# Kernel tuning notes

Hardware: AMD Instinct MI355X
Metric: run time of the kernel (lower is better)

Reference implementation:

```python
import jax, jax.numpy as jnp
import numpy as np

B, S, D = 8, 2048, 1024
TEMPERATURE = 32.0  # sqrt(d_model)
NEG_INF = -1e16


def setup_inputs() -> dict:
    key = jax.random.key(0)
    ks = jax.random.split(key, 9)
    sc = 1.0 / np.sqrt(D)
    q = jax.random.normal(ks[0], (B, S, D), dtype=jnp.float32)
    k = jax.random.normal(ks[1], (B, S, D), dtype=jnp.float32)
    v = jax.random.normal(ks[2], (B, S, D), dtype=jnp.float32)
    # nn.Linear weights are [out, in]; init roughly uniform(-1/sqrt(in), 1/sqrt(in))
    Wq = jax.random.uniform(ks[3], (D, D), jnp.float32, -sc, sc)
    Wk = jax.random.uniform(ks[4], (D, D), jnp.float32, -sc, sc)
    Wv = jax.random.uniform(ks[5], (D, D), jnp.float32, -sc, sc)
    bq = jax.random.uniform(ks[6], (D,), jnp.float32, -sc, sc)
    bk = jax.random.uniform(ks[7], (D,), jnp.float32, -sc, sc)
    bv = jax.random.uniform(ks[8], (D,), jnp.float32, -sc, sc)
    # causal mask: True where attention is DISALLOWED (masked_fill semantics)
    mask = jnp.triu(jnp.ones((S, S), dtype=bool), k=1)
    mask = jnp.broadcast_to(mask[None, :, :], (B, S, S))
    return {"q": q, "k": k, "v": v, "Wq": Wq, "bq": bq, "Wk": Wk,
            "bk": bk, "Wv": Wv, "bv": bv, "mask": mask}


def reference(q, k, v, Wq, bq, Wk, bk, Wv, bv, mask):
    # Linear projections (torch Linear: x @ W.T + b)
    qp = jnp.einsum('bsd,ed->bse', q, Wq) + bq  # [B,S,D]
    kp = jnp.einsum('bsd,ed->bse', k, Wk) + bk
    vp = jnp.einsum('bsd,ed->bse', v, Wv) + bv
    # scores [B,S,S]
    attn = jnp.einsum('bsd,btd->bst', qp, kp) / TEMPERATURE
    attn = jnp.where(mask, NEG_INF, attn)
    attn = jax.nn.softmax(attn, axis=2)
    # dropout p=0.0 -> identity (eval mode)
    output = jnp.einsum('bst,btd->bsd', attn, vp)  # [B,S,D]
    return (output, attn)
```

## Files before the change

### kernel.cpp

```cpp
#include <hip/hip_runtime.h>
#include <hip/hip_bf16.h>
#include <stdint.h>

#define SEQ 2048
#define DIM 1024
#define NB  8

typedef __attribute__((ext_vector_type(8))) __bf16 bf16x8;
typedef __attribute__((ext_vector_type(8))) unsigned short ushort8;
typedef __attribute__((ext_vector_type(4))) float f32x4;

__device__ inline unsigned short f2b(float f) {
  union { float f; uint32_t u; } c; c.f = f;
  uint32_t u = c.u;
  return (unsigned short)((u + 0x7fffu + ((u >> 16) & 1u)) >> 16);
}

__device__ inline void async16(const void* g, void* l) {
  __builtin_amdgcn_global_load_lds((const __attribute__((address_space(1))) uint32_t*)g,
                                   (__attribute__((address_space(3))) uint32_t*)l,
                                   16, 0, 0);
}

__global__ __launch_bounds__(256) void cvt_f32_bf16(const float* __restrict__ in,
                                                    unsigned short* __restrict__ out, int n4) {
  int idx = blockIdx.x * 256 + threadIdx.x;
  int stride = gridDim.x * 256;
  for (int i = idx; i < n4; i += stride) {
    float4 f = ((const float4*)in)[i];
    ushort4 h;
    h.x = f2b(f.x); h.y = f2b(f.y); h.z = f2b(f.z); h.w = f2b(f.w);
    ((ushort4*)out)[i] = h;
  }
}

template<int MODE>
__global__ __launch_bounds__(512, 2)
void gemm256(const unsigned short* __restrict__ A,
             const unsigned short* __restrict__ B,
             void* __restrict__ Cv,
             const float* __restrict__ bias,
             int K, int lda, int ldb, int ldc,
             long long aStride, long long bStride, long long cStride,
             float scale)
{
  extern __shared__ __align__(16) unsigned short lds[];
  unsigned short* const lA0 = lds;
  unsigned short* const lB0 = lds + 4 * 8192;

  const int mT = gridDim.x, nT = gridDim.y;
  const int nwg = mT * nT;
  const int did = blockIdx.y * mT + blockIdx.x;
  const int chunk = nwg >> 3;
  const int tile = (did & 7) * chunk + (did >> 3);
  const int bm = tile / nT;
  const int bn = tile % nT;
  if (MODE == 1 && bn > bm) return;
  const int bm0 = bm << 8;
  const int bn0 = bn << 8;
  const int z = blockIdx.z;
  A += (long long)z * aStride;
  B += (long long)z * bStride;

  const int tid  = threadIdx.x;
  const int lane = tid & 63;
  const int wv   = tid >> 6;
  const int wm   = wv >> 2;
  const int wn   = wv & 3;
  const int l15  = lane & 15;
  const int l4   = lane >> 4;
  const int Keff = (MODE == 2) ? (bm0 + 256) : K;
  const int NT   = Keff >> 6;

  auto LAh = [&](int buf, int kh) { return lA0 + ((buf << 1) + kh) * 8192; };
  auto LBh = [&](int buf, int kh) { return lB0 + ((buf << 1) + kh) * 8192; };

  const int rS   = tid >> 2;
  const int cSrc = ((tid & 3) << 4) ^ ((rS & 3) << 4);
  const char* gA0 = (const char*)A + ((size_t)(bm0 + rS) * lda) * 2 + cSrc;
  const char* gA1 = gA0 + (size_t)128 * lda * 2;
  const char* gB0 = (const char*)B + ((size_t)(bn0 + rS) * ldb) * 2 + cSrc;
  const char* gB1 = gB0 + (size_t)128 * ldb * 2;

  auto stageA = [&](int buf, int t64, int kh) {
    size_t ko = (size_t)t64 * 128 + (size_t)(kh << 6);
    unsigned short* d = LAh(buf, kh);
    async16(gA0 + ko, d + tid * 8);
    async16(gA1 + ko, d + (tid + 512) * 8);
  };
  auto stageB = [&](int buf, int t64, int kh) {
    size_t ko = (size_t)t64 * 128 + (size_t)(kh << 6);
    unsigned short* d = LBh(buf, kh);
    async16(gB0 + ko, d + tid * 8);
    async16(gB1 + ko, d + (tid + 512) * 8);
  };

  const int swz = (l4 << 4) ^ ((l15 & 3) << 4);
  int aOff[8], bOff[4];
  #pragma unroll
  for (int m = 0; m < 8; ++m) aOff[m] = ((wm << 7) + (m << 4) + l15) * 64 + swz;
  #pragma unroll
  for (int n = 0; n < 4; ++n) bOff[n] = ((wn << 6) + (n << 4) + l15) * 64 + swz;

  auto rd = [&](const unsigned short* base, int off) -> bf16x8 {
    return __builtin_bit_cast(bf16x8, *(const ushort8*)((const char*)base + off));
  };

  f32x4 acc[8][4] = {};
  bf16x8 aF[8], bFa, bFb;

  stageA(0, 0, 0); stageB(0, 0, 0); stageA(0, 0, 1); stageB(0, 0, 1);
  stageA(1, 1, 0); stageB(1, 1, 0); stageA(1, 1, 1);
  asm volatile("s_waitcnt vmcnt(6)" ::: "memory");
  __builtin_amdgcn_s_barrier();
  __builtin_amdgcn_sched_barrier(0);

  for (int tt = 0; tt < NT; ++tt) {
    const int buf = tt & 1;
    const unsigned short* a0 = LAh(buf, 0);
    const unsigned short* a1 = LAh(buf, 1);
    const unsigned short* b0 = LBh(buf, 0);
    const unsigned short* b1 = LBh(buf, 1);

    #pragma unroll
    for (int m = 0; m < 8; ++m) aF[m] = rd(a0, aOff[m]);
    bFa = rd(b0, bOff[0]); bFb = rd(b0, bOff[1]);
    if (tt + 1 < NT) stageB(buf ^ 1, tt + 1, 1);
    __builtin_amdgcn_s_barrier();
    asm volatile("s_waitcnt lgkmcnt(0)" ::: "memory");
    __builtin_amdgcn_sched_barrier(0);
    __builtin_amdgcn_s_setprio(1);
    #pragma unroll
    for (int m = 0; m < 8; ++m) {
      acc[m][0] = __builtin_amdgcn_mfma_f32_16x16x32_bf16(aF[m], bFa, acc[m][0], 0, 0, 0);
      acc[m][1] = __builtin_amdgcn_mfma_f32_16x16x32_bf16(aF[m], bFb, acc[m][1], 0, 0, 0);
    }
    __builtin_amdgcn_s_setprio(0);
    __builtin_amdgcn_s_barrier();
    __builtin_amdgcn_sched_barrier(0);

    bFa = rd(b0, bOff[2]); bFb = rd(b0, bOff[3]);
    if (tt + 2 < NT) stageA(buf, tt + 2, 0);
    __builtin_amdgcn_s_barrier();
    asm volatile("s_waitcnt lgkmcnt(0)" ::: "memory");
    __builtin_amdgcn_sched_barrier(0);
    __builtin_amdgcn_s_setprio(1);
    #pragma unroll
    for (int m = 0; m < 8; ++m) {
      acc[m][2] = __builtin_amdgcn_mfma_f32_16x16x32_bf16(aF[m], bFa, acc[m][2], 0, 0, 0);
      acc[m][3] = __builtin_amdgcn_mfma_f32_16x16x32_bf16(aF[m], bFb, acc[m][3], 0, 0, 0);
    }
    __builtin_amdgcn_s_setprio(0);
    __builtin_amdgcn_s_barrier();
    __builtin_amdgcn_sched_barrier(0);

    #pragma unroll
    for (int m = 0; m < 8; ++m) aF[m] = rd(a1, aOff[m]);
    bFa = rd(b1, bOff[0]); bFb = rd(b1, bOff[1]);
    if (tt + 2 < NT) stageB(buf, tt + 2, 0);
    __builtin_amdgcn_s_barrier();
    asm volatile("s_waitcnt lgkmcnt(0)" ::: "memory");
    __builtin_amdgcn_sched_barrier(0);
    __builtin_amdgcn_s_setprio(1);
    #pragma unroll
    for (int m = 0; m < 8; ++m) {
      acc[m][0] = __builtin_amdgcn_mfma_f32_16x16x32_bf16(aF[m], bFa, acc[m][0], 0, 0, 0);
      acc[m][1] = __builtin_amdgcn_mfma_f32_16x16x32_bf16(aF[m], bFb, acc[m][1], 0, 0, 0);
    }
    __builtin_amdgcn_s_setprio(0);
    __builtin_amdgcn_s_barrier();
    __builtin_amdgcn_sched_barrier(0);

    bFa = rd(b1, bOff[2]); bFb = rd(b1, bOff[3]);
    if (tt + 2 < NT) stageA(buf, tt + 2, 1);
    __builtin_amdgcn_s_barrier();
    asm volatile("s_waitcnt lgkmcnt(0)" ::: "memory");
    __builtin_amdgcn_sched_barrier(0);
    __builtin_amdgcn_s_setprio(1);
    #pragma unroll
    for (int m = 0; m < 8; ++m) {
      acc[m][2] = __builtin_amdgcn_mfma_f32_16x16x32_bf16(aF[m], bFa, acc[m][2], 0, 0, 0);
      acc[m][3] = __builtin_amdgcn_mfma_f32_16x16x32_bf16(aF[m], bFb, acc[m][3], 0, 0, 0);
    }
    __builtin_amdgcn_s_setprio(0);
    if (tt + 2 < NT) asm volatile("s_waitcnt vmcnt(6)" ::: "memory");
    else             asm volatile("s_waitcnt vmcnt(0)" ::: "memory");
    __builtin_amdgcn_s_barrier();
    __builtin_amdgcn_sched_barrier(0);
  }

  if (MODE == 0) {
    unsigned short* Ch = (unsigned short*)Cv;
    float bvv[4];
    #pragma unroll
    for (int n = 0; n < 4; ++n) bvv[n] = bias[bn0 + (wn << 6) + (n << 4) + l15];
    #pragma unroll
    for (int m = 0; m < 8; ++m) {
      int rowb = bm0 + (wm << 7) + (m << 4) + (l4 << 2);
      #pragma unroll
      for (int r = 0; r < 4; ++r) {
        int row = rowb + r;
        #pragma unroll
        for (int n = 0; n < 4; ++n) {
          int col = bn0 + (wn << 6) + (n << 4) + l15;
          Ch[(size_t)row * ldc + col] = f2b(acc[m][n][r] + bvv[n]);
        }
      }
    }
  } else {
    float* Cf = (float*)Cv + (long long)z * cStride;
    #pragma unroll
    for (int m = 0; m < 8; ++m) {
      int rowb = bm0 + (wm << 7) + (m << 4) + (l4 << 2);
      #pragma unroll
      for (int r = 0; r < 4; ++r) {
        int row = rowb + r;
        #pragma unroll
        for (int n = 0; n < 4; ++n) {
          int col = bn0 + (wn << 6) + (n << 4) + l15;
          Cf[(size_t)row * ldc + col] = acc[m][n][r] * scale;
        }
      }
    }
  }
}

__global__ __launch_bounds__(256)
void softmax_causal(float* __restrict__ attnF, unsigned short* __restrict__ attnH) {
  const int S = SEQ;
  int row = blockIdx.x;
  int i = row & (S - 1);
  float* rp = attnF + (size_t)row * S;
  unsigned short* hp = attnH + (size_t)row * S;
  int len = i + 1;
  int tid = threadIdx.x;
  float vals[8];
  float m = -1e30f;
  #pragma unroll
  for (int it = 0; it < 8; ++it) {
    int j = it * 256 + tid;
    float v = (j < len) ? rp[j] : -1e30f;
    vals[it] = v;
    m = fmaxf(m, v);
  }
  #pragma unroll
  for (int o = 32; o > 0; o >>= 1) m = fmaxf(m, __shfl_xor(m, o, 64));
  __shared__ float red[4];
  int wv = tid >> 6, lane = tid & 63;
  if (lane == 0) red[wv] = m;
  __syncthreads();
  m = fmaxf(fmaxf(red[0], red[1]), fmaxf(red[2], red[3]));
  __syncthreads();
  float s = 0.f;
  #pragma unroll
  for (int it = 0; it < 8; ++it) {
    float e = __expf(vals[it] - m);
    vals[it] = e;
    s += e;
  }
  #pragma unroll
  for (int o = 32; o > 0; o >>= 1) s += __shfl_xor(s, o, 64);
  if (lane == 0) red[wv] = s;
  __syncthreads();
  s = red[0] + red[1] + red[2] + red[3];
  float inv = 1.f / s;
  #pragma unroll
  for (int it = 0; it < 8; ++it) {
    float o = vals[it] * inv;
    rp[it * 256 + tid] = o;
    hp[it * 256 + tid] = f2b(o);
  }
}

__global__ void transpose_bf16(const unsigned short* __restrict__ in, unsigned short* __restrict__ out) {
  __shared__ unsigned short tile[32][33];
  size_t zoff = (size_t)blockIdx.z * SEQ * DIM;
  const unsigned short* ip = in + zoff;
  unsigned short* op = out + zoff;
  int c0 = blockIdx.x * 32;
  int r0 = blockIdx.y * 32;
  int tx = threadIdx.x, ty = threadIdx.y;
  #pragma unroll
  for (int dy = 0; dy < 32; dy += 8)
    tile[ty + dy][tx] = ip[(size_t)(r0 + ty + dy) * DIM + c0 + tx];
  __syncthreads();
  #pragma unroll
  for (int dy = 0; dy < 32; dy += 8)
    op[(size_t)(c0 + ty + dy) * SEQ + r0 + tx] = tile[tx][ty + dy];
}

extern "C" void kernel_launch(void* const* d_in, const int* in_sizes, int n_in,
                              void* d_out, int out_size, void* d_ws, size_t ws_size,
                              hipStream_t stream) {
  (void)in_sizes; (void)n_in; (void)out_size; (void)ws_size;
  const int B = NB, S = SEQ, D = DIM;
  const size_t BSD = (size_t)B * S * D;
  const size_t DD  = (size_t)D * D;

  const float* q  = (const float*)d_in[0];
  const float* k  = (const float*)d_in[1];
  const float* v  = (const float*)d_in[2];
  const float* Wq = (const float*)d_in[3];
  const float* bq = (const float*)d_in[4];
  const float* Wk = (const float*)d_in[5];
  const float* bk = (const float*)d_in[6];
  const float* Wv = (const float*)d_in[7];
  const float* bv = (const float*)d_in[8];

  float* out   = (float*)d_out;
  float* attnF = out + BSD;

  unsigned short* xb  = (unsigned short*)d_ws;
  unsigned short* Wqb = xb + BSD;
  unsigned short* Wkb = Wqb + DD;
  unsigned short* Wvb = Wkb + DD;
  unsigned short* qp  = Wvb + DD;
  unsigned short* kp  = qp + BSD;
  unsigned short* vp  = kp + BSD;
  unsigned short* attnH = vp;

  static bool attrDone = []() {
    hipFuncSetAttribute(reinterpret_cast<const void*>(&gemm256<0>),
                        hipFuncAttributeMaxDynamicSharedMemorySize, 131072);
    hipFuncSetAttribute(reinterpret_cast<const void*>(&gemm256<1>),
                        hipFuncAttributeMaxDynamicSharedMemorySize, 131072);
    hipFuncSetAttribute(reinterpret_cast<const void*>(&gemm256<2>),
                        hipFuncAttributeMaxDynamicSharedMemorySize, 131072);
    return true;
  }();
  (void)attrDone;

  dim3 blk(256);
  dim3 gblk(512);
  const size_t GLDS = 131072;
  cvt_f32_bf16<<<dim3(512), blk, 0, stream>>>(Wq, Wqb, (int)(DD / 4));
  cvt_f32_bf16<<<dim3(512), blk, 0, stream>>>(Wk, Wkb, (int)(DD / 4));
  cvt_f32_bf16<<<dim3(512), blk, 0, stream>>>(Wv, Wvb, (int)(DD / 4));
  cvt_f32_bf16<<<dim3(4096), blk, 0, stream>>>(q, xb, (int)(BSD / 4));
  gemm256<0><<<dim3(64, 4, 1), gblk, GLDS, stream>>>(xb, Wqb, qp, bq, D, D, D, D, 0, 0, 0, 1.f);
  cvt_f32_bf16<<<dim3(4096), blk, 0, stream>>>(k, xb, (int)(BSD / 4));
  gemm256<0><<<dim3(64, 4, 1), gblk, GLDS, stream>>>(xb, Wkb, kp, bk, D, D, D, D, 0, 0, 0, 1.f);
  cvt_f32_bf16<<<dim3(4096), blk, 0, stream>>>(v, xb, (int)(BSD / 4));
  gemm256<0><<<dim3(64, 4, 1), gblk, GLDS, stream>>>(xb, Wvb, vp, bv, D, D, D, D, 0, 0, 0, 1.f);
  transpose_bf16<<<dim3(D / 32, S / 32, B), dim3(32, 8), 0, stream>>>(vp, xb);
  gemm256<1><<<dim3(S / 256, S / 256, B), gblk, GLDS, stream>>>(qp, kp, attnF, nullptr,
      D, D, D, S, (long long)S * D, (long long)S * D, (long long)S * S, 1.f / 32.f);
  softmax_causal<<<dim3(B * S), blk, 0, stream>>>(attnF, attnH);
  gemm256<2><<<dim3(S / 256, D / 256, B), gblk, GLDS, stream>>>(attnH, xb, out, nullptr,
      S, S, S, D, (long long)S * S, (long long)D * S, (long long)S * D, 1.f);
}
```

Before: 729.7 us.

## Batch QKV projections into one launch, restructure GEMM LDS reads, vectorize transpose

Merges the three weight conversions and the three input conversions into grid-y batched kernels. The three QKV projection GEMMs become a single z-batched launch with a per-z bias, provided the workspace is large enough. The GEMM inner loop now loads all four B fragments at once, dropping two of the four barrier/lgkmcnt wait points per k-step. The V transpose moves to 64x64 tiles with 16-byte vector accesses and an XOR-swizzled LDS tile. A fallback path keeps sequential projections for small workspaces. The tradeoffs are more registers per thread in the GEMM and a larger workspace requirement.

```diff
diff --git a/kernel.cpp b/kernel.cpp
--- a/kernel.cpp
+++ b/kernel.cpp
@@ -34,12 +34,30 @@
   }
 }
 
+__global__ __launch_bounds__(256) void cvt3_f32_bf16(const float* __restrict__ s0,
+                                                     const float* __restrict__ s1,
+                                                     const float* __restrict__ s2,
+                                                     unsigned short* __restrict__ out, int n4) {
+  const float* src = (blockIdx.y == 0) ? s0 : (blockIdx.y == 1) ? s1 : s2;
+  unsigned short* dst = out + (size_t)blockIdx.y * (size_t)n4 * 4;
+  int idx = blockIdx.x * 256 + threadIdx.x;
+  int stride = gridDim.x * 256;
+  for (int i = idx; i < n4; i += stride) {
+    float4 f = ((const float4*)src)[i];
+    ushort4 h;
+    h.x = f2b(f.x); h.y = f2b(f.y); h.z = f2b(f.z); h.w = f2b(f.w);
+    ((ushort4*)dst)[i] = h;
+  }
+}
+
 template<int MODE>
 __global__ __launch_bounds__(512, 2)
 void gemm256(const unsigned short* __restrict__ A,
              const unsigned short* __restrict__ B,
              void* __restrict__ Cv,
-             const float* __restrict__ bias,
+             const float* __restrict__ bias0,
+             const float* __restrict__ bias1,
+             const float* __restrict__ bias2,
              int K, int lda, int ldb, int ldc,
              long long aStride, long long bStride, long long cStride,
              float scale)
@@ -107,7 +125,7 @@
   };
 
   f32x4 acc[8][4] = {};
-  bf16x8 aF[8], bFa, bFb;
+  bf16x8 aF[8], bF[4];
 
   stageA(0, 0, 0); stageB(0, 0, 0); stageA(0, 0, 1); stageB(0, 0, 1);
   stageA(1, 1, 0); stageB(1, 1, 0); stageA(1, 1, 1);
@@ -124,7 +142,8 @@
 
     #pragma unroll
     for (int m = 0; m < 8; ++m) aF[m] = rd(a0, aOff[m]);
-    bFa = rd(b0, bOff[0]); bFb = rd(b0, bOff[1]);
+    #pragma unroll
+    for (int n = 0; n < 4; ++n) bF[n] = rd(b0, bOff[n]);
     if (tt + 1 < NT) stageB(buf ^ 1, tt + 1, 1);
     __builtin_amdgcn_s_barrier();
     asm volatile("s_waitcnt lgkmcnt(0)" ::: "memory");
@@ -132,55 +151,48 @@
     __builtin_amdgcn_s_setprio(1);
     #pragma unroll
     for (int m = 0; m < 8; ++m) {
-      acc[m][0] = __builtin_amdgcn_mfma_f32_16x16x32_bf16(aF[m], bFa, acc[m][0], 0, 0, 0);
-      acc[m][1] = __builtin_amdgcn_mfma_f32_16x16x32_bf16(aF[m], bFb, acc[m][1], 0, 0, 0);
+      acc[m][0] = __builtin_amdgcn_mfma_f32_16x16x32_bf16(aF[m], bF[0], acc[m][0], 0, 0, 0);
+      acc[m][1] = __builtin_amdgcn_mfma_f32_16x16x32_bf16(aF[m], bF[1], acc[m][1], 0, 0, 0);
     }
     __builtin_amdgcn_s_setprio(0);
     __builtin_amdgcn_s_barrier();
     __builtin_amdgcn_sched_barrier(0);
 
-    bFa = rd(b0, bOff[2]); bFb = rd(b0, bOff[3]);
     if (tt + 2 < NT) stageA(buf, tt + 2, 0);
+    __builtin_amdgcn_s_setprio(1);
+    #pragma unroll
+    for (int m = 0; m < 8; ++m) {
+      acc[m][2] = __builtin_amdgcn_mfma_f32_16x16x32_bf16(aF[m], bF[2], acc[m][2], 0, 0, 0);
+      acc[m][3] = __builtin_amdgcn_mfma_f32_16x16x32_bf16(aF[m], bF[3], acc[m][3], 0, 0, 0);
+    }
+    __builtin_amdgcn_s_setprio(0);
+    __builtin_amdgcn_s_barrier();
+    __builtin_amdgcn_sched_barrier(0);
+
+    #pragma unroll
+    for (int m = 0; m < 8; ++m) aF[m] = rd(a1, aOff[m]);
+    #pragma unroll
+    for (int n = 0; n < 4; ++n) bF[n] = rd(b1, bOff[n]);
+    if (tt + 2 < NT) stageB(buf, tt + 2, 0);
     __builtin_amdgcn_s_barrier();
     asm volatile("s_waitcnt lgkmcnt(0)" ::: "memory");
     __builtin_amdgcn_sched_barrier(0);
     __builtin_amdgcn_s_setprio(1);
     #pragma unroll
     for (int m = 0; m < 8; ++m) {
-      acc[m][2] = __builtin_amdgcn_mfma_f32_16x16x32_bf16(aF[m], bFa, acc[m][2], 0, 0, 0);
-      acc[m][3] = __builtin_amdgcn_mfma_f32_16x16x32_bf16(aF[m], bFb, acc[m][3], 0, 0, 0);
+      acc[m][0] = __builtin_amdgcn_mfma_f32_16x16x32_bf16(aF[m], bF[0], acc[m][0], 0, 0, 0);
+      acc[m][1] = __builtin_amdgcn_mfma_f32_16x16x32_bf16(aF[m], bF[1], acc[m][1], 0, 0, 0);
     }
     __builtin_amdgcn_s_setprio(0);
     __builtin_amdgcn_s_barrier();
     __builtin_amdgcn_sched_barrier(0);
 
-    #pragma unroll
-    for (int m = 0; m < 8; ++m) aF[m] = rd(a1, aOff[m]);
-    bFa = rd(b1, bOff[0]); bFb = rd(b1, bOff[1]);
-    if (tt + 2 < NT) stageB(buf, tt + 2, 0);
-    __builtin_amdgcn_s_barrier();
-    asm volatile("s_waitcnt lgkmcnt(0)" ::: "memory");
-    __builtin_amdgcn_sched_barrier(0);
+    if (tt + 2 < NT) stageA(buf, tt + 2, 1);
     __builtin_amdgcn_s_setprio(1);
     #pragma unroll
     for (int m = 0; m < 8; ++m) {
-      acc[m][0] = __builtin_amdgcn_mfma_f32_16x16x32_bf16(aF[m], bFa, acc[m][0], 0, 0, 0);
-      acc[m][1] = __builtin_amdgcn_mfma_f32_16x16x32_bf16(aF[m], bFb, acc[m][1], 0, 0, 0);
-    }
-    __builtin_amdgcn_s_setprio(0);
-    __builtin_amdgcn_s_barrier();
-    __builtin_amdgcn_sched_barrier(0);
-
-    bFa = rd(b1, bOff[2]); bFb = rd(b1, bOff[3]);
-    if (tt + 2 < NT) stageA(buf, tt + 2, 1);
-    __builtin_amdgcn_s_barrier();
-    asm volatile("s_waitcnt lgkmcnt(0)" ::: "memory");
-    __builtin_amdgcn_sched_barrier(0);
-    __builtin_amdgcn_s_setprio(1);
-    #pragma unroll
-    for (int m = 0; m < 8; ++m) {
-      acc[m][2] = __builtin_amdgcn_mfma_f32_16x16x32_bf16(aF[m], bFa, acc[m][2], 0, 0, 0);
-      acc[m][3] = __builtin_amdgcn_mfma_f32_16x16x32_bf16(aF[m], bFb, acc[m][3], 0, 0, 0);
+      acc[m][2] = __builtin_amdgcn_mfma_f32_16x16x32_bf16(aF[m], bF[2], acc[m][2], 0, 0, 0);
+      acc[m][3] = __builtin_amdgcn_mfma_f32_16x16x32_bf16(aF[m], bF[3], acc[m][3], 0, 0, 0);
     }
     __builtin_amdgcn_s_setprio(0);
     if (tt + 2 < NT) asm volatile("s_waitcnt vmcnt(6)" ::: "memory");
@@ -190,10 +202,11 @@
   }
 
   if (MODE == 0) {
-    unsigned short* Ch = (unsigned short*)Cv;
+    unsigned short* Ch = (unsigned short*)Cv + (long long)z * cStride;
+    const float* bp = (z == 0) ? bias0 : (z == 1) ? bias1 : bias2;
     float bvv[4];
     #pragma unroll
-    for (int n = 0; n < 4; ++n) bvv[n] = bias[bn0 + (wn << 6) + (n << 4) + l15];
+    for (int n = 0; n < 4; ++n) bvv[n] = bp[bn0 + (wn << 6) + (n << 4) + l15];
     #pragma unroll
     for (int m = 0; m < 8; ++m) {
       int rowb = bm0 + (wm << 7) + (m << 4) + (l4 << 2);
@@ -272,29 +285,46 @@
   }
 }
 
-__global__ void transpose_bf16(const unsigned short* __restrict__ in, unsigned short* __restrict__ out) {
-  __shared__ unsigned short tile[32][33];
+__global__ __launch_bounds__(256)
+void transpose64_bf16(const unsigned short* __restrict__ in, unsigned short* __restrict__ out) {
+  __shared__ unsigned short tile[64][72];
   size_t zoff = (size_t)blockIdx.z * SEQ * DIM;
   const unsigned short* ip = in + zoff;
   unsigned short* op = out + zoff;
-  int c0 = blockIdx.x * 32;
-  int r0 = blockIdx.y * 32;
-  int tx = threadIdx.x, ty = threadIdx.y;
-  #pragma unroll
-  for (int dy = 0; dy < 32; dy += 8)
-    tile[ty + dy][tx] = ip[(size_t)(r0 + ty + dy) * DIM + c0 + tx];
+  int c0 = blockIdx.x * 64;
+  int r0 = blockIdx.y * 64;
+  int tid = threadIdx.x;
+  #pragma unroll
+  for (int p = 0; p < 2; ++p) {
+    int e = tid + p * 256;
+    int row = e >> 3;
+    int cv  = (e & 7) << 3;
+    ushort8 v = *(const ushort8*)&ip[(size_t)(r0 + row) * DIM + c0 + cv];
+    #pragma unroll
+    for (int j = 0; j < 8; ++j) {
+      int c = cv + j;
+      tile[c][row ^ (((c >> 3) & 7) << 3)] = v[j];
+    }
+  }
   __syncthreads();
   #pragma unroll
-  for (int dy = 0; dy < 32; dy += 8)
-    op[(size_t)(c0 + ty + dy) * SEQ + r0 + tx] = tile[tx][ty + dy];
+  for (int p = 0; p < 2; ++p) {
+    int e = tid + p * 256;
+    int orow = e >> 3;
+    int ocv  = (e & 7) << 3;
+    int osw  = ocv ^ (((orow >> 3) & 7) << 3);
+    ushort8 v = *(const ushort8*)&tile[orow][osw];
+    *(ushort8*)&op[(size_t)(c0 + orow) * SEQ + r0 + ocv] = v;
+  }
 }
 
 extern "C" void kernel_launch(void* const* d_in, const int* in_sizes, int n_in,
                               void* d_out, int out_size, void* d_ws, size_t ws_size,
                               hipStream_t stream) {
-  (void)in_sizes; (void)n_in; (void)out_size; (void)ws_size;
+  (void)in_sizes; (void)n_in; (void)out_size;
   const int B = NB, S = SEQ, D = DIM;
   const size_t BSD = (size_t)B * S * D;
+  const size_t BSS = (size_t)B * S * S;
   const size_t DD  = (size_t)D * D;
 
   const float* q  = (const float*)d_in[0];
@@ -309,15 +339,6 @@
 
   float* out   = (float*)d_out;
   float* attnF = out + BSD;
-
-  unsigned short* xb  = (unsigned short*)d_ws;
-  unsigned short* Wqb = xb + BSD;
-  unsigned short* Wkb = Wqb + DD;
-  unsigned short* Wvb = Wkb + DD;
-  unsigned short* qp  = Wvb + DD;
-  unsigned short* kp  = qp + BSD;
-  unsigned short* vp  = kp + BSD;
-  unsigned short* attnH = vp;
 
   static bool attrDone = []() {
     hipFuncSetAttribute(reinterpret_cast<const void*>(&gemm256<0>),
@@ -333,19 +354,58 @@
   dim3 blk(256);
   dim3 gblk(512);
   const size_t GLDS = 131072;
-  cvt_f32_bf16<<<dim3(512), blk, 0, stream>>>(Wq, Wqb, (int)(DD / 4));
-  cvt_f32_bf16<<<dim3(512), blk, 0, stream>>>(Wk, Wkb, (int)(DD / 4));
-  cvt_f32_bf16<<<dim3(512), blk, 0, stream>>>(Wv, Wvb, (int)(DD / 4));
-  cvt_f32_bf16<<<dim3(4096), blk, 0, stream>>>(q, xb, (int)(BSD / 4));
-  gemm256<0><<<dim3(64, 4, 1), gblk, GLDS, stream>>>(xb, Wqb, qp, bq, D, D, D, D, 0, 0, 0, 1.f);
-  cvt_f32_bf16<<<dim3(4096), blk, 0, stream>>>(k, xb, (int)(BSD / 4));
-  gemm256<0><<<dim3(64, 4, 1), gblk, GLDS, stream>>>(xb, Wkb, kp, bk, D, D, D, D, 0, 0, 0, 1.f);
-  cvt_f32_bf16<<<dim3(4096), blk, 0, stream>>>(v, xb, (int)(BSD / 4));
-  gemm256<0><<<dim3(64, 4, 1), gblk, GLDS, stream>>>(xb, Wvb, vp, bv, D, D, D, D, 0, 0, 0, 1.f);
-  transpose_bf16<<<dim3(D / 32, S / 32, B), dim3(32, 8), 0, stream>>>(vp, xb);
-  gemm256<1><<<dim3(S / 256, S / 256, B), gblk, GLDS, stream>>>(qp, kp, attnF, nullptr,
-      D, D, D, S, (long long)S * D, (long long)S * D, (long long)S * S, 1.f / 32.f);
-  softmax_causal<<<dim3(B * S), blk, 0, stream>>>(attnF, attnH);
-  gemm256<2><<<dim3(S / 256, D / 256, B), gblk, GLDS, stream>>>(attnH, xb, out, nullptr,
-      S, S, S, D, (long long)S * S, (long long)D * S, (long long)S * D, 1.f);
-}
+
+  const size_t needBig = (5 * BSD + 3 * DD + BSS) * 2;
+  if (ws_size >= needBig) {
+    unsigned short* qb  = (unsigned short*)d_ws;
+    unsigned short* kb  = qb + BSD;
+    unsigned short* vb  = kb + BSD;
+    unsigned short* Wqb = vb + BSD;
+    unsigned short* qp  = Wqb + 3 * DD;
+    unsigned short* kp  = qp + BSD;
+    unsigned short* vp  = kp + BSD;
+    unsigned short* attnH = vp;
+    unsigned short* vpT = qb;
+
+    cvt3_f32_bf16<<<dim3(512, 3), blk, 0, stream>>>(Wq, Wk, Wv, Wqb, (int)(DD / 4));
+    cvt3_f32_bf16<<<dim3(4096, 3), blk, 0, stream>>>(q, k, v, qb, (int)(BSD / 4));
+    gemm256<0><<<dim3(64, 4, 3), gblk, GLDS, stream>>>(qb, Wqb, qp, bq, bk, bv,
+        D, D, D, D, (long long)BSD, (long long)DD, (long long)BSD, 1.f);
+    transpose64_bf16<<<dim3(D / 64, S / 64, B), blk, 0, stream>>>(vp, vpT);
+    gemm256<1><<<dim3(S / 256, S / 256, B), gblk, GLDS, stream>>>(qp, kp, attnF,
+        nullptr, nullptr, nullptr,
+        D, D, D, S, (long long)S * D, (long long)S * D, (long long)S * S, 1.f / 32.f);
+    softmax_causal<<<dim3(B * S), blk, 0, stream>>>(attnF, attnH);
+    gemm256<2><<<dim3(S / 256, D / 256, B), gblk, GLDS, stream>>>(attnH, vpT, out,
+        nullptr, nullptr, nullptr,
+        S, S, S, D, (long long)S * S, (long long)D * S, (long long)S * D, 1.f);
+  } else {
+    unsigned short* xb  = (unsigned short*)d_ws;
+    unsigned short* Wqb = xb + BSD;
+    unsigned short* Wkb = Wqb + DD;
+    unsigned short* Wvb = Wkb + DD;
+    unsigned short* qp  = Wvb + DD;
+    unsigned short* kp  = qp + BSD;
+    unsigned short* vp  = kp + BSD;
+    unsigned short* attnH = vp;
+
+    cvt3_f32_bf16<<<dim3(512, 3), blk, 0, stream>>>(Wq, Wk, Wv, Wqb, (int)(DD / 4));
+    cvt_f32_bf16<<<dim3(4096), blk, 0, stream>>>(q, xb, (int)(BSD / 4));
+    gemm256<0><<<dim3(64, 4, 1), gblk, GLDS, stream>>>(xb, Wqb, qp, bq, bq, bq,
+        D, D, D, D, 0, 0, 0, 1.f);
+    cvt_f32_bf16<<<dim3(4096), blk, 0, stream>>>(k, xb, (int)(BSD / 4));
+    gemm256<0><<<dim3(64, 4, 1), gblk, GLDS, stream>>>(xb, Wqb + DD, kp, bk, bk, bk,
+        D, D, D, D, 0, 0, 0, 1.f);
+    cvt_f32_bf16<<<dim3(4096), blk, 0, stream>>>(v, xb, (int)(BSD / 4));
+    gemm256<0><<<dim3(64, 4, 1), gblk, GLDS, stream>>>(xb, Wvb, vp, bv, bv, bv,
+        D, D, D, D, 0, 0, 0, 1.f);
+    transpose64_bf16<<<dim3(D / 64, S / 64, B), blk, 0, stream>>>(vp, xb);
+    gemm256<1><<<dim3(S / 256, S / 256, B), gblk, GLDS, stream>>>(qp, kp, attnF,
+        nullptr, nullptr, nullptr,
+        D, D, D, S, (long long)S * D, (long long)S * D, (long long)S * S, 1.f / 32.f);
+    softmax_causal<<<dim3(B * S), blk, 0, stream>>>(attnF, attnH);
+    gemm256<2><<<dim3(S / 256, D / 256, B), gblk, GLDS, stream>>>(attnH, xb, out,
+        nullptr, nullptr, nullptr,
+        S, S, S, D, (long long)S * S, (long long)D * S, (long long)S * D, 1.f);
+  }
+}
```

Measured after the change: 725.9 us. Within noise of the previous version (-0.5%).
